# Performance work log

Hardware: AMD Instinct MI355X
Metric: run time of the kernel (lower is better)

The kernel has to match this reference:

```python
import jax, jax.numpy as jnp
import numpy as np

H = 512
B, T = 16, 600
LN_EPS = 1e-5


def _lstm_dir(x, w_ih, w_hh, b, reverse):
    # x: [B,T,In], w_ih: [4H,In], w_hh: [4H,H], b: [4H] (b_ih+b_hh combined)
    if reverse:
        x = jnp.flip(x, axis=1)
    xp = jnp.einsum('bti,gi->btg', x, w_ih) + b  # [B,T,4H] gate preactivations from input
    h0 = jnp.zeros((x.shape[0], w_hh.shape[1]), x.dtype)
    c0 = jnp.zeros_like(h0)

    def step(carry, g_t):
        h, c = carry
        g = g_t + h @ w_hh.T
        i, f, gg, o = jnp.split(g, 4, axis=-1)  # torch gate order: i,f,g,o
        i = jax.nn.sigmoid(i)
        f = jax.nn.sigmoid(f)
        gg = jnp.tanh(gg)
        o = jax.nn.sigmoid(o)
        c = f * c + i * gg
        h = o * jnp.tanh(c)
        return (h, c), h

    _, hs = jax.lax.scan(step, (h0, c0), jnp.swapaxes(xp, 0, 1))
    hs = jnp.swapaxes(hs, 0, 1)  # [B,T,H]
    if reverse:
        hs = jnp.flip(hs, axis=1)
    return hs


def setup_inputs() -> dict:
    key = jax.random.key(0)
    ks = jax.random.split(key, 20)
    s = 1.0 / np.sqrt(H)
    u = lambda k, shape: jax.random.uniform(k, shape, jnp.float32, -s, s)
    inp = {'x': jax.random.normal(ks[0], (B, H, T), jnp.float32)}
    # layer 0: input H; layer 1: input 2H (bidirectional concat)
    inp['w_ih_l0f'] = u(ks[1], (4 * H, H));     inp['w_hh_l0f'] = u(ks[2], (4 * H, H));  inp['b_l0f'] = u(ks[3], (4 * H,))
    inp['w_ih_l0b'] = u(ks[4], (4 * H, H));     inp['w_hh_l0b'] = u(ks[5], (4 * H, H));  inp['b_l0b'] = u(ks[6], (4 * H,))
    inp['w_ih_l1f'] = u(ks[7], (4 * H, 2 * H)); inp['w_hh_l1f'] = u(ks[8], (4 * H, H));  inp['b_l1f'] = u(ks[9], (4 * H,))
    inp['w_ih_l1b'] = u(ks[10], (4 * H, 2 * H)); inp['w_hh_l1b'] = u(ks[11], (4 * H, H)); inp['b_l1b'] = u(ks[12], (4 * H,))
    inp['fc_w'] = u(ks[13], (H, 2 * H))
    inp['fc_b'] = u(ks[14], (H,))
    inp['ln_w'] = jnp.ones((H,), jnp.float32)
    inp['ln_b'] = jnp.zeros((H,), jnp.float32)
    return inp


def reference(x, w_ih_l0f, w_hh_l0f, b_l0f, w_ih_l0b, w_hh_l0b, b_l0b,
              w_ih_l1f, w_hh_l1f, b_l1f, w_ih_l1b, w_hh_l1b, b_l1b,
              fc_w, fc_b, ln_w, ln_b):
    xt = jnp.transpose(x, (0, 2, 1))  # [B,T,H]
    # layer 0 (bi)
    h0f = _lstm_dir(xt, w_ih_l0f, w_hh_l0f, b_l0f, False)
    h0b = _lstm_dir(xt, w_ih_l0b, w_hh_l0b, b_l0b, True)
    h0 = jnp.concatenate([h0f, h0b], axis=-1)  # [B,T,2H]
    # layer 1 (bi)
    h1f = _lstm_dir(h0, w_ih_l1f, w_hh_l1f, b_l1f, False)
    h1b = _lstm_dir(h0, w_ih_l1b, w_hh_l1b, b_l1b, True)
    h1 = jnp.concatenate([h1f, h1b], axis=-1)  # [B,T,2H]
    # fc -> layernorm -> relu
    out = jnp.einsum('btk,hk->bth', h1, fc_w) + fc_b
    mu = jnp.mean(out, axis=-1, keepdims=True)
    var = jnp.mean(jnp.square(out - mu), axis=-1, keepdims=True)
    out = (out - mu) * jax.lax.rsqrt(var + LN_EPS) * ln_w + ln_b
    return jax.nn.relu(out)
```

## Files before the change

### kernel.cpp

```cpp
#include <hip/hip_runtime.h>
#include <hip/hip_bf16.h>

#define HDIM 512
#define BATCH 16
#define TSEQ 600
#define NROW (BATCH*TSEQ)

typedef unsigned short u16;
typedef unsigned long long u64;
typedef __attribute__((ext_vector_type(8))) short short8;
typedef __attribute__((ext_vector_type(4))) float f32x4;
typedef __attribute__((ext_vector_type(4))) int i32x4;

__device__ __forceinline__ u16 f2b(float f){
  unsigned x; __builtin_memcpy(&x, &f, 4);
  x += 0x7fffu + ((x >> 16) & 1u);
  return (u16)(x >> 16);
}
__device__ __forceinline__ float b2f(u16 u){
  unsigned x = ((unsigned)u) << 16; float f; __builtin_memcpy(&f, &x, 4); return f;
}

#define LOG2E 1.44269504f
__device__ __forceinline__ float fsig(float x){
  return __builtin_amdgcn_rcpf(1.f + __builtin_amdgcn_exp2f(-x*LOG2E));
}
__device__ __forceinline__ float ftanh(float x){
  return 2.f*__builtin_amdgcn_rcpf(1.f + __builtin_amdgcn_exp2f(-2.f*LOG2E*x)) - 1.f;
}

__global__ void cvt_kernel(const float* __restrict__ in, u16* __restrict__ out, int n4){
  int i = blockIdx.x*blockDim.x + threadIdx.x;
  if (i < n4){
    float4 v = ((const float4*)in)[i];
    ushort4 u; u.x=f2b(v.x); u.y=f2b(v.y); u.z=f2b(v.z); u.w=f2b(v.w);
    ((ushort4*)out)[i] = u;
  }
}

__global__ void maxabs_kernel(const float* __restrict__ in, unsigned* __restrict__ outmax, int n){
  float m = 0.f;
  for (int i = blockIdx.x*blockDim.x + threadIdx.x; i < n; i += gridDim.x*blockDim.x)
    m = fmaxf(m, fabsf(in[i]));
  for (int off=32; off>0; off>>=1) m = fmaxf(m, __shfl_down(m, off));
  if ((threadIdx.x & 63) == 0) atomicMax(outmax, __float_as_uint(m));
}

__global__ void quantw_kernel(const float* __restrict__ in, const unsigned* __restrict__ maxu,
                              signed char* __restrict__ out, int n4){
  int i = blockIdx.x*blockDim.x + threadIdx.x;
  if (i >= n4) return;
  float s = 127.f / fmaxf(__uint_as_float(*maxu), 1e-20f);
  float4 v = ((const float4*)in)[i];
  unsigned a = (unsigned)((int)rintf(v.x*s) & 255);
  unsigned b = (unsigned)((int)rintf(v.y*s) & 255);
  unsigned c = (unsigned)((int)rintf(v.z*s) & 255);
  unsigned d = (unsigned)((int)rintf(v.w*s) & 255);
  ((unsigned*)out)[i] = a | (b<<8) | (c<<16) | (d<<24);
}

__global__ __launch_bounds__(256) void transpose_kernel(const float* __restrict__ x, u16* __restrict__ xt){
  __shared__ float tile[32][33];
  int t0 = blockIdx.x*32, h0 = blockIdx.y*32, b = blockIdx.z;
  int li = threadIdx.x & 31, lj = threadIdx.x >> 5;
  for (int j=lj; j<32; j+=8){
    int t = t0 + li;
    tile[j][li] = (t < TSEQ) ? x[((size_t)b*HDIM + h0 + j)*TSEQ + t] : 0.f;
  }
  __syncthreads();
  for (int j=lj; j<32; j+=8){
    int t = t0 + j;
    if (t < TSEQ) xt[((size_t)b*TSEQ + t)*HDIM + h0 + li] = f2b(tile[li][j]);
  }
}

template<typename OT>
__global__ __launch_bounds__(256) void gemm_bt(const u16* __restrict__ A, const u16* __restrict__ B,
    const float* __restrict__ bias, OT* __restrict__ C, int M, int N, int K)
{
  __shared__ u16 As[128][40];
  __shared__ u16 Bs[128][40];
  const int m0 = blockIdx.x*128, n0 = blockIdx.y*128;
  const int tid = threadIdx.x, lane = tid & 63;
  const int wr = ((tid>>6)&1)*64, wc = ((tid>>6)>>1)*64;
  const int srow = tid>>2, scol = (tid&3)*8;
  f32x4 acc[4][4] = {};
  for (int k0=0; k0<K; k0+=32){
    uint4 a0 = *(const uint4*)(A + (size_t)(m0+srow)*K    + k0 + scol);
    uint4 a1 = *(const uint4*)(A + (size_t)(m0+srow+64)*K + k0 + scol);
    uint4 b0 = *(const uint4*)(B + (size_t)(n0+srow)*K    + k0 + scol);
    uint4 b1 = *(const uint4*)(B + (size_t)(n0+srow+64)*K + k0 + scol);
    __syncthreads();
    *(uint4*)&As[srow][scol]    = a0;
    *(uint4*)&As[srow+64][scol] = a1;
    *(uint4*)&Bs[srow][scol]    = b0;
    *(uint4*)&Bs[srow+64][scol] = b1;
    __syncthreads();
    short8 af[4], bfr[4];
#pragma unroll
    for (int i=0;i<4;i++) af[i]  = *(const short8*)&As[wr + i*16 + (lane&15)][(lane>>4)*8];
#pragma unroll
    for (int i=0;i<4;i++) bfr[i] = *(const short8*)&Bs[wc + i*16 + (lane&15)][(lane>>4)*8];
#pragma unroll
    for (int i=0;i<4;i++)
#pragma unroll
      for (int j=0;j<4;j++)
        acc[i][j] = __builtin_amdgcn_mfma_f32_16x16x32_bf16(af[i], bfr[j], acc[i][j], 0,0,0);
  }
#pragma unroll
  for (int i=0;i<4;i++)
#pragma unroll
    for (int j=0;j<4;j++){
      int row = m0 + wr + i*16 + (lane>>4)*4;
      int col = n0 + wc + j*16 + (lane&15);
      float bv = bias ? bias[col] : 0.f;
#pragma unroll
      for (int r=0;r<4;r++){
        float v = acc[i][j][r] + bv;
        if (sizeof(OT) == 2) C[(size_t)(row+r)*N + col] = (OT)f2b(v);
        else                 C[(size_t)(row+r)*N + col] = (OT)v;
      }
    }
}

__global__ __launch_bounds__(512, 1) void lstm_rec8(
    const u16* __restrict__ xp_f, const u16* __restrict__ xp_b,
    const signed char* __restrict__ w8_f, const signed char* __restrict__ w8_b,
    const unsigned* __restrict__ maxu,
    u16* __restrict__ h_out,
    unsigned char* __restrict__ ppl,
    unsigned* __restrict__ tags)
{
  const int bi = blockIdx.x, rem = bi & 7;
  if (rem > 1) return;
  const int dir = rem, wid = bi >> 3;
  const int tid = threadIdx.x, lane = tid & 63, w = tid >> 6;
  const int l15 = lane & 15, lq = lane >> 4;
  const int P = wid*128 + w*16;

  const u16* xp = dir ? xp_b : xp_f;
  const signed char* w8 = dir ? w8_b : w8_f;
  const float mx = __uint_as_float(maxu[dir]);
  const float sA = mx / (127.f*127.f);

  __shared__ __align__(16) signed char hL[2][16][528];

  i32x4 wf[4][8];
#pragma unroll
  for (int g=0; g<4; ++g)
#pragma unroll
    for (int kk=0; kk<8; ++kk)
      wf[g][kk] = *(const i32x4*)(w8 + (size_t)(g*512 + P + l15)*512 + kk*64 + lq*16);

  float c[4] = {0.f,0.f,0.f,0.f};
  const int t0 = dir ? (TSEQ-1) : 0, ts = dir ? -1 : 1;

  for (int s=0; s<TSEQ; ++s){
    const int t = t0 + s*ts;
    const int par = s & 1;

    ushort4 xq[4];
    {
      const u16* px = xp + ((size_t)(l15*TSEQ + t))*2048 + P + lq*4;
#pragma unroll
      for (int g=0; g<4; ++g) xq[g] = *(const ushort4*)(px + g*512);
    }

    if (tid < 32){
      const unsigned* tp = tags + ((dir*2 + par)*32 + tid)*4;
      while ((int)__hip_atomic_load(tp, __ATOMIC_RELAXED, __HIP_MEMORY_SCOPE_AGENT) < s) {}
    }
    __syncthreads();

    {
      const u64* src = (const u64*)(ppl + (size_t)(dir*2 + par)*8192);
      int b = tid >> 5, p16 = tid & 31;
      const u64* q = src + b*64 + p16*2;
      u64 lo = __hip_atomic_load(q,   __ATOMIC_RELAXED, __HIP_MEMORY_SCOPE_AGENT);
      u64 hi = __hip_atomic_load(q+1, __ATOMIC_RELAXED, __HIP_MEMORY_SCOPE_AGENT);
      *(u64*)&hL[par][b][p16*16]     = lo;
      *(u64*)&hL[par][b][p16*16 + 8] = hi;
    }
    __syncthreads();

    i32x4 acc[4] = {};
#pragma unroll
    for (int kk=0; kk<8; ++kk){
      i32x4 b1 = *(const i32x4*)(&hL[par][l15][0] + kk*64 + lq*16);
#pragma unroll
      for (int g=0; g<4; ++g)
        acc[g] = __builtin_amdgcn_mfma_i32_16x16x64_i8(wf[g][kk], b1, acc[g], 0, 0, 0);
    }

    unsigned pk1 = 0; float hhv[4];
#pragma unroll
    for (int r=0; r<4; ++r){
      float pre[4];
#pragma unroll
      for (int g=0; g<4; ++g)
        pre[g] = b2f(((const u16*)&xq[g])[r]) + sA*(float)acc[g][r];
      float iv = fsig(pre[0]);
      float fv = fsig(pre[1]);
      float gv = ftanh(pre[2]);
      float ov = fsig(pre[3]);
      float cc = fv*c[r] + iv*gv; c[r] = cc;
      float hh = ov*ftanh(cc);
      hhv[r] = hh;
      int d1i = (int)rintf(hh*127.f);
      pk1 |= (unsigned)(d1i & 255) << (8*r);
    }
    if (s < TSEQ-1){
      unsigned* pd = (unsigned*)(ppl + (size_t)(dir*2 + (par^1))*8192) + ((l15*512 + P + lq*4) >> 2);
      __hip_atomic_store(pd, pk1, __ATOMIC_RELAXED, __HIP_MEMORY_SCOPE_AGENT);
      asm volatile("s_waitcnt vmcnt(0)" ::: "memory");
      if (lane == 0){
        unsigned* tg = tags + ((dir*2 + (par^1))*32 + wid*8 + w)*4;
        __hip_atomic_store(tg, (unsigned)(s+1), __ATOMIC_RELAXED, __HIP_MEMORY_SCOPE_AGENT);
      }
    }
    ushort4 hu;
#pragma unroll
    for (int r=0; r<4; ++r) ((u16*)&hu)[r] = f2b(hhv[r]);
    *(ushort4*)(h_out + ((size_t)(l15*TSEQ + t))*1024 + dir*512 + P + lq*4) = hu;
  }
}

__global__ __launch_bounds__(256) void ln_relu_kernel(const float* __restrict__ in,
    const float* __restrict__ gw, const float* __restrict__ gb, float* __restrict__ out)
{
  __shared__ float rs[4], rss[4];
  const int row = blockIdx.x;
  const float* p = in + (size_t)row*HDIM;
  float v0 = p[threadIdx.x], v1 = p[threadIdx.x + 256];
  float s = v0 + v1, ss = v0*v0 + v1*v1;
  for (int off=32; off>0; off>>=1){
    s  += __shfl_down(s, off);
    ss += __shfl_down(ss, off);
  }
  if ((threadIdx.x & 63) == 0){ rs[threadIdx.x>>6] = s; rss[threadIdx.x>>6] = ss; }
  __syncthreads();
  float st  = rs[0]+rs[1]+rs[2]+rs[3];
  float sst = rss[0]+rss[1]+rss[2]+rss[3];
  float mu  = st * (1.f/HDIM);
  float var = sst * (1.f/HDIM) - mu*mu;
  float rstd = rsqrtf(var + 1e-5f);
  int c0 = threadIdx.x, c1 = threadIdx.x + 256;
  float y0 = (v0 - mu)*rstd*gw[c0] + gb[c0];
  float y1 = (v1 - mu)*rstd*gw[c1] + gb[c1];
  out[(size_t)row*HDIM + c0] = fmaxf(y0, 0.f);
  out[(size_t)row*HDIM + c1] = fmaxf(y1, 0.f);
}

extern "C" void kernel_launch(void* const* d_in, const int* in_sizes, int n_in,
                              void* d_out, int out_size, void* d_ws, size_t ws_size,
                              hipStream_t stream)
{
  const float* x        = (const float*)d_in[0];
  const float* wih_l0f  = (const float*)d_in[1];
  const float* whh_l0f  = (const float*)d_in[2];
  const float* b_l0f    = (const float*)d_in[3];
  const float* wih_l0b  = (const float*)d_in[4];
  const float* whh_l0b  = (const float*)d_in[5];
  const float* b_l0b    = (const float*)d_in[6];
  const float* wih_l1f  = (const float*)d_in[7];
  const float* whh_l1f  = (const float*)d_in[8];
  const float* b_l1f    = (const float*)d_in[9];
  const float* wih_l1b  = (const float*)d_in[10];
  const float* whh_l1b  = (const float*)d_in[11];
  const float* b_l1b    = (const float*)d_in[12];
  const float* fc_w     = (const float*)d_in[13];
  const float* fc_b     = (const float*)d_in[14];
  const float* ln_w     = (const float*)d_in[15];
  const float* ln_b     = (const float*)d_in[16];
  float* outp = (float*)d_out;

  char* base = (char*)d_ws;
  size_t off = 0;
  auto alloc = [&](size_t bytes)->char*{ char* p = base + off; off += (bytes + 255) & ~(size_t)255; return p; };

  unsigned* maxu = (unsigned*)alloc(256);
  unsigned char* ppl0 = (unsigned char*)alloc((size_t)2*2*8192);
  unsigned char* ppl1 = (unsigned char*)alloc((size_t)2*2*8192);
  unsigned* tags0 = (unsigned*)alloc((size_t)2*2*32*16);
  unsigned* tags1 = (unsigned*)alloc((size_t)2*2*32*16);
  size_t zero_bytes = off;
  signed char* w8_l0f = (signed char*)alloc((size_t)2048*512);
  signed char* w8_l0b = (signed char*)alloc((size_t)2048*512);
  signed char* w8_l1f = (signed char*)alloc((size_t)2048*512);
  signed char* w8_l1b = (signed char*)alloc((size_t)2048*512);
  u16* xt     = (u16*)alloc((size_t)NROW*512*2);
  u16* wb_l0f = (u16*)alloc((size_t)2048*512*2);
  u16* wb_l0b = (u16*)alloc((size_t)2048*512*2);
  u16* wb_l1f = (u16*)alloc((size_t)2048*1024*2);
  u16* wb_l1b = (u16*)alloc((size_t)2048*1024*2);
  u16* wb_fc  = (u16*)alloc((size_t)512*1024*2);
  u16* h0     = (u16*)alloc((size_t)NROW*1024*2);
  u16* h1     = (u16*)alloc((size_t)NROW*1024*2);
  u16* xpf    = (u16*)alloc((size_t)NROW*2048*2);
  u16* xpb    = (u16*)alloc((size_t)NROW*2048*2);
  float* fco  = (float*)alloc((size_t)NROW*512*4);
  (void)ws_size; (void)in_sizes; (void)n_in; (void)out_size;

  hipMemsetAsync(d_ws, 0, zero_bytes, stream);

  auto cvt = [&](const float* in, u16* out, int n){
    int n4 = n/4;
    cvt_kernel<<<dim3((n4+255)/256), 256, 0, stream>>>(in, out, n4);
  };
  cvt(wih_l0f, wb_l0f, 2048*512);
  cvt(wih_l0b, wb_l0b, 2048*512);
  cvt(wih_l1f, wb_l1f, 2048*1024);
  cvt(wih_l1b, wb_l1b, 2048*1024);
  cvt(fc_w,    wb_fc,  512*1024);

  maxabs_kernel<<<dim3(256), 256, 0, stream>>>(whh_l0f, maxu+0, 2048*512);
  maxabs_kernel<<<dim3(256), 256, 0, stream>>>(whh_l0b, maxu+1, 2048*512);
  maxabs_kernel<<<dim3(256), 256, 0, stream>>>(whh_l1f, maxu+2, 2048*512);
  maxabs_kernel<<<dim3(256), 256, 0, stream>>>(whh_l1b, maxu+3, 2048*512);
  quantw_kernel<<<dim3((2048*512/4+255)/256), 256, 0, stream>>>(whh_l0f, maxu+0, w8_l0f, 2048*512/4);
  quantw_kernel<<<dim3((2048*512/4+255)/256), 256, 0, stream>>>(whh_l0b, maxu+1, w8_l0b, 2048*512/4);
  quantw_kernel<<<dim3((2048*512/4+255)/256), 256, 0, stream>>>(whh_l1f, maxu+2, w8_l1f, 2048*512/4);
  quantw_kernel<<<dim3((2048*512/4+255)/256), 256, 0, stream>>>(whh_l1b, maxu+3, w8_l1b, 2048*512/4);

  transpose_kernel<<<dim3(19,16,16), 256, 0, stream>>>(x, xt);

  gemm_bt<u16><<<dim3(75,16), 256, 0, stream>>>(xt, wb_l0f, b_l0f, xpf, NROW, 2048, 512);
  gemm_bt<u16><<<dim3(75,16), 256, 0, stream>>>(xt, wb_l0b, b_l0b, xpb, NROW, 2048, 512);
  lstm_rec8<<<dim3(32), 512, 0, stream>>>(xpf, xpb, w8_l0f, w8_l0b, maxu+0, h0, ppl0, tags0);

  gemm_bt<u16><<<dim3(75,16), 256, 0, stream>>>(h0, wb_l1f, b_l1f, xpf, NROW, 2048, 1024);
  gemm_bt<u16><<<dim3(75,16), 256, 0, stream>>>(h0, wb_l1b, b_l1b, xpb, NROW, 2048, 1024);
  lstm_rec8<<<dim3(32), 512, 0, stream>>>(xpf, xpb, w8_l1f, w8_l1b, maxu+2, h1, ppl1, tags1);

  gemm_bt<float><<<dim3(75,4), 256, 0, stream>>>(h1, wb_fc, fc_b, fco, NROW, 512, 1024);
  ln_relu_kernel<<<dim3(NROW), 256, 0, stream>>>(fco, ln_w, ln_b, outp);
}
```

Before: 4.088 ms.

## Embed step tags in 64-bit hidden-state chunks to remove separate flag handshake

```diff
diff --git a/kernel.cpp b/kernel.cpp
--- a/kernel.cpp
+++ b/kernel.cpp
@@ -123,13 +123,12 @@
     }
 }
 
-__global__ __launch_bounds__(512, 1) void lstm_rec8(
+__global__ __launch_bounds__(512, 1) void lstm_rec9(
     const u16* __restrict__ xp_f, const u16* __restrict__ xp_b,
     const signed char* __restrict__ w8_f, const signed char* __restrict__ w8_b,
     const unsigned* __restrict__ maxu,
     u16* __restrict__ h_out,
-    unsigned char* __restrict__ ppl,
-    unsigned* __restrict__ tags)
+    u64* __restrict__ dpl)
 {
   const int bi = blockIdx.x, rem = bi & 7;
   if (rem > 1) return;
@@ -152,6 +151,12 @@
     for (int kk=0; kk<8; ++kk)
       wf[g][kk] = *(const i32x4*)(w8 + (size_t)(g*512 + P + l15)*512 + kk*64 + lq*16);
 
+  u64* pl = dpl + (size_t)dir*(2*2048);
+  const int mychunk = l15*128 + (P >> 2) + lq;
+  const int cb = tid >> 5, cp16 = tid & 31;
+  const int cP = (cp16 >> 3)*128 + (cp16 & 7)*16;
+  const int coff = cb*128 + (cP >> 2);
+
   float c[4] = {0.f,0.f,0.f,0.f};
   const int t0 = dir ? (TSEQ-1) : 0, ts = dir ? -1 : 1;
 
@@ -166,20 +171,26 @@
       for (int g=0; g<4; ++g) xq[g] = *(const ushort4*)(px + g*512);
     }
 
-    if (tid < 32){
-      const unsigned* tp = tags + ((dir*2 + par)*32 + tid)*4;
-      while ((int)__hip_atomic_load(tp, __ATOMIC_RELAXED, __HIP_MEMORY_SCOPE_AGENT) < s) {}
-    }
-    __syncthreads();
-
     {
-      const u64* src = (const u64*)(ppl + (size_t)(dir*2 + par)*8192);
-      int b = tid >> 5, p16 = tid & 31;
-      const u64* q = src + b*64 + p16*2;
-      u64 lo = __hip_atomic_load(q,   __ATOMIC_RELAXED, __HIP_MEMORY_SCOPE_AGENT);
-      u64 hi = __hip_atomic_load(q+1, __ATOMIC_RELAXED, __HIP_MEMORY_SCOPE_AGENT);
-      *(u64*)&hL[par][b][p16*16]     = lo;
-      *(u64*)&hL[par][b][p16*16 + 8] = hi;
+      const u64* q = pl + (size_t)par*2048 + coff;
+      u64 v[4];
+#pragma unroll
+      for (int i=0;i<4;i++)
+        v[i] = __hip_atomic_load(q+i, __ATOMIC_RELAXED, __HIP_MEMORY_SCOPE_AGENT);
+      for (;;){
+        bool ok = true;
+#pragma unroll
+        for (int i=0;i<4;i++) ok &= ((unsigned)(v[i] >> 32) == (unsigned)s);
+        if (ok) break;
+#pragma unroll
+        for (int i=0;i<4;i++)
+          if ((unsigned)(v[i] >> 32) != (unsigned)s)
+            v[i] = __hip_atomic_load(q+i, __ATOMIC_RELAXED, __HIP_MEMORY_SCOPE_AGENT);
+      }
+      u64 lo = (u64)(unsigned)v[0] | ((u64)(unsigned)v[1] << 32);
+      u64 hi = (u64)(unsigned)v[2] | ((u64)(unsigned)v[3] << 32);
+      *(u64*)&hL[par][cb][cP]     = lo;
+      *(u64*)&hL[par][cb][cP + 8] = hi;
     }
     __syncthreads();
 
@@ -210,13 +221,9 @@
       pk1 |= (unsigned)(d1i & 255) << (8*r);
     }
     if (s < TSEQ-1){
-      unsigned* pd = (unsigned*)(ppl + (size_t)(dir*2 + (par^1))*8192) + ((l15*512 + P + lq*4) >> 2);
-      __hip_atomic_store(pd, pk1, __ATOMIC_RELAXED, __HIP_MEMORY_SCOPE_AGENT);
-      asm volatile("s_waitcnt vmcnt(0)" ::: "memory");
-      if (lane == 0){
-        unsigned* tg = tags + ((dir*2 + (par^1))*32 + wid*8 + w)*4;
-        __hip_atomic_store(tg, (unsigned)(s+1), __ATOMIC_RELAXED, __HIP_MEMORY_SCOPE_AGENT);
-      }
+      u64 chunk = ((u64)(unsigned)(s+1) << 32) | (u64)pk1;
+      __hip_atomic_store(pl + (size_t)(par^1)*2048 + mychunk, chunk,
+                         __ATOMIC_RELAXED, __HIP_MEMORY_SCOPE_AGENT);
     }
     ushort4 hu;
 #pragma unroll
@@ -279,10 +286,8 @@
   auto alloc = [&](size_t bytes)->char*{ char* p = base + off; off += (bytes + 255) & ~(size_t)255; return p; };
 
   unsigned* maxu = (unsigned*)alloc(256);
-  unsigned char* ppl0 = (unsigned char*)alloc((size_t)2*2*8192);
-  unsigned char* ppl1 = (unsigned char*)alloc((size_t)2*2*8192);
-  unsigned* tags0 = (unsigned*)alloc((size_t)2*2*32*16);
-  unsigned* tags1 = (unsigned*)alloc((size_t)2*2*32*16);
+  u64* dpl0 = (u64*)alloc((size_t)2*2*2048*8);
+  u64* dpl1 = (u64*)alloc((size_t)2*2*2048*8);
   size_t zero_bytes = off;
   signed char* w8_l0f = (signed char*)alloc((size_t)2048*512);
   signed char* w8_l0b = (signed char*)alloc((size_t)2048*512);
@@ -326,11 +331,11 @@
 
   gemm_bt<u16><<<dim3(75,16), 256, 0, stream>>>(xt, wb_l0f, b_l0f, xpf, NROW, 2048, 512);
   gemm_bt<u16><<<dim3(75,16), 256, 0, stream>>>(xt, wb_l0b, b_l0b, xpb, NROW, 2048, 512);
-  lstm_rec8<<<dim3(32), 512, 0, stream>>>(xpf, xpb, w8_l0f, w8_l0b, maxu+0, h0, ppl0, tags0);
+  lstm_rec9<<<dim3(32), 512, 0, stream>>>(xpf, xpb, w8_l0f, w8_l0b, maxu+0, h0, dpl0);
 
   gemm_bt<u16><<<dim3(75,16), 256, 0, stream>>>(h0, wb_l1f, b_l1f, xpf, NROW, 2048, 1024);
   gemm_bt<u16><<<dim3(75,16), 256, 0, stream>>>(h0, wb_l1b, b_l1b, xpb, NROW, 2048, 1024);
-  lstm_rec8<<<dim3(32), 512, 0, stream>>>(xpf, xpb, w8_l1f, w8_l1b, maxu+2, h1, ppl1, tags1);
+  lstm_rec9<<<dim3(32), 512, 0, stream>>>(xpf, xpb, w8_l1f, w8_l1b, maxu+2, h1, dpl1);
 
   gemm_bt<float><<<dim3(75,4), 256, 0, stream>>>(h1, wb_fc, fc_b, fco, NROW, 512, 1024);
   ln_relu_kernel<<<dim3(NROW), 256, 0, stream>>>(fco, ln_w, ln_b, outp);
```

Result: slower. 4.534 ms (+10.9%).
